# Kernel optimization log

Hardware: AMD Instinct MI355X
Metric: run time of the kernel (lower is better)

The kernel has to match this reference:

```python
import math
import jax, jax.numpy as jnp
import numpy as np

LOG2_E = math.log2(math.e)
C = 64          # channels
N = 150_000     # coarse-level occupied nodes
CHILD = 4       # occupied children per node (static => M is static)
M = N * CHILD   # fine-level points
K = 27          # 3x3x3 sparse-conv kernel offsets


def _prelu(x, a):
    return jnp.where(x >= 0, x, a * x)


def _sparse_conv(x, nbr, mask, W, b):
    """MinkowskiConvolution(k=3): y[i] = sum_k mask[i,k] * x[nbr[i,k]] @ W[k] + b.
    Fixed loop over K=27 offsets keeps peak memory at [n, C] per step."""
    y = jnp.zeros((x.shape[0], W.shape[2]), x.dtype)
    for k in range(W.shape[0]):
        g = x[nbr[:, k]] * mask[:, k, None]
        y = y + g @ W[k]
    return y + b


def setup_inputs() -> dict:
    rng = np.random.default_rng(0)
    # exactly CHILD occupied children per parent -> static M
    mask1 = np.argsort(rng.random((N, 8)), axis=1) < CHILD   # [N, 8] bool
    sel_idx = np.flatnonzero(mask1.reshape(-1)).astype(np.int32)  # [M]
    bins1_f = mask1.astype(np.float32)
    bins0 = rng.random((M, 8)) < 0.5
    bins0[:, 0] |= ~bins0.any(1)   # octree node has >=1 occupied child => label in [0,254]

    def nbrs(n):
        nb = rng.integers(0, n, size=(n, K)).astype(np.int32)
        mk = rng.random((n, K)) < 0.6
        nb[:, K // 2] = np.arange(n)  # center offset is self
        mk[:, K // 2] = True
        return nb, mk

    nbr0, mask0 = nbrs(N)
    nbr1, mask1k = nbrs(M)

    key = jax.random.key(0)
    ks = jax.random.split(key, 12)
    w = lambda k, sh, fan: (jax.random.normal(k, sh, jnp.float32) / np.sqrt(fan))
    params = dict(
        W_dec=w(ks[0], (C + 8, C), C + 8), b_dec=jnp.zeros((C,), jnp.float32), a_dec=jnp.float32(0.25),
        Wb1=w(ks[1], (K, C, C), K * C), bb1=jnp.zeros((C,), jnp.float32), ab1=jnp.float32(0.25),
        Wb2=w(ks[2], (K, C, C), K * C), bb2=jnp.zeros((C,), jnp.float32), ab2=jnp.float32(0.25),
        Wp0=w(ks[3], (K, C, C), K * C), bp0=jnp.zeros((C,), jnp.float32), ap0=jnp.float32(0.25),
        Wl0=w(ks[4], (C, 8 * C), C), bl0=jnp.zeros((8 * C,), jnp.float32),
        Wp1=w(ks[5], (K, C, C), K * C), bp1=jnp.zeros((C,), jnp.float32), ap1=jnp.float32(0.25),
        Wl1=w(ks[6], (C, 255), C), bl1=jnp.zeros((255,), jnp.float32),
    )
    return dict(
        cur_rec_F=jax.random.normal(ks[7], (N, C), jnp.float32),
        bins1_f=jnp.asarray(bins1_f), bins0=jnp.asarray(bins0),
        sel_idx=jnp.asarray(sel_idx),
        nbr0=jnp.asarray(nbr0), mask0=jnp.asarray(mask0),
        nbr1=jnp.asarray(nbr1), mask1=jnp.asarray(mask1k),
        points_num=M,
        **params,
    )


def reference(cur_rec_F, bins1_f, bins0, sel_idx, nbr0, mask0, nbr1, mask1, points_num,
              W_dec, b_dec, a_dec, Wb1, bb1, ab1, Wb2, bb2, ab2,
              Wp0, bp0, ap0, Wl0, bl0, Wp1, bp1, ap1, Wl1, bl1):
    # embed (pred_steps==2): identity on cur_bins[1].F
    embed_f = bins1_f                                   # [N, 8]
    # dec: Linear(C+8 -> C) + PReLU + Block(C)
    x = _prelu(jnp.concatenate([cur_rec_F, embed_f], 1) @ W_dec + b_dec, a_dec)
    h = _prelu(_sparse_conv(x, nbr0, mask0, Wb1, bb1), ab1)
    h = _sparse_conv(h, nbr0, mask0, Wb2, bb2) + x      # residual add (x.F.add_)
    rec = _prelu(h, ab2)                                # [N, C] -> cur_rec output
    # pred[0]: Conv3 + PReLU + Linear(C -> 8C)
    p = _prelu(_sparse_conv(rec, nbr0, mask0, Wp0, bp0), ap0)
    p = p @ Wl0 + bl0                                   # [N, 8C]
    # gather occupied children: reshape(N,8,C)[bins1] with static selection indices
    tmp = p.reshape(-1, p.shape[1] // 8)[sel_idx]       # [M, C]
    # pred[1] (last): Conv3 + PReLU + Linear(C -> 255) at finer stride
    q = _prelu(_sparse_conv(tmp, nbr1, mask1, Wp1, bp1), ap1)
    logits = q @ Wl1 + bl1                              # [M, 255]
    # bit-pack octree labels: (bins0 << arange(8)).sum(1) - 1
    oct = jnp.sum(bins0.astype(jnp.int32) * (1 << jnp.arange(8, dtype=jnp.int32)), 1) - 1
    logp = jax.nn.log_softmax(logits, axis=-1)
    ce = -jnp.take_along_axis(logp, oct[:, None], axis=1).sum()
    loss = ce * (LOG2_E / points_num)                   # batch_size==1 branch
    return rec, loss
```

## Files before the change

### kernel.cpp

```cpp
#include <hip/hip_runtime.h>
#include <hip/hip_bf16.h>

typedef __attribute__((ext_vector_type(8))) short bf16x8;
typedef __attribute__((ext_vector_type(4))) float f32x4;

#define MFMA(a,b,c) __builtin_amdgcn_mfma_f32_16x16x32_bf16(a,b,c,0,0,0)

__device__ __forceinline__ short f2b(float v){
  __hip_bfloat16 b = __float2bfloat16(v);
  return *reinterpret_cast<short*>(&b);
}
__device__ __forceinline__ float b2f(short s){
  __hip_bfloat16 b;
  *reinterpret_cast<short*>(&b) = s;
  return __bfloat162float(b);
}
__device__ __forceinline__ bool rd_mask(const void* m, long i, int flag){
  if (flag==1) return ((const int*)m)[i] != 0;
  if (flag==2) return ((const float*)m)[i] != 0.0f;
  return ((const unsigned char*)m)[i] != 0;
}

__device__ __forceinline__ void gld16(const void* g, void* l){
  __builtin_amdgcn_global_load_lds(
      (const __attribute__((address_space(1))) unsigned int*)g,
      (__attribute__((address_space(3))) unsigned int*)l, 16, 0, 0);
}
__device__ __forceinline__ void gld4(const void* g, void* l){
  __builtin_amdgcn_global_load_lds(
      (const __attribute__((address_space(1))) unsigned int*)g,
      (__attribute__((address_space(3))) unsigned int*)l, 4, 0, 0);
}

__global__ void k_detect(const void* __restrict__ mask, int* flag, float* ce,
                         int* zrow){
  int t = threadIdx.x;
  if (t < 32 && blockIdx.x==0) zrow[t] = 0;
  if (t==0 && blockIdx.x==0){
    const int* mi = (const int*)mask;
    const float* mf = (const float*)mask;
    bool all_i=true, all_f=true;
    for (int i=0;i<100;i++){
      if (mi[i*27+13] != 1) all_i=false;
      if (mf[i*27+13] != 1.0f) all_f=false;
    }
    *flag = all_i ? 1 : (all_f ? 2 : 0);
    *ce = 0.0f;
  }
}

__global__ __launch_bounds__(256) void k_merge(int* __restrict__ nbr,
    const void* __restrict__ mask, int total, const int* __restrict__ flagp){
  int flag = *flagp;
  int i = blockIdx.x*256 + threadIdx.x;
  if (i < total && !rd_mask(mask, i, flag)) nbr[i] = -1;
}

__global__ __launch_bounds__(256) void k_prep(
    const float* __restrict__ Wdec, const float* __restrict__ Wb1,
    const float* __restrict__ Wb2, const float* __restrict__ Wp0,
    const float* __restrict__ Wp1, const float* __restrict__ Wl0,
    const float* __restrict__ Wl1,
    short* __restrict__ wdecf, short* __restrict__ wconvf,
    short* __restrict__ wl0f, short* __restrict__ wl1f)
{
  int i = blockIdx.x*256 + threadIdx.x;
  if (i < 442368){
    int ci = i / 110592, r = i % 110592;
    int e = r&7, ln=(r>>3)&63, ks=(r>>9)&1, ct=(r>>10)&3, k=r>>12;
    int cin = ks*32 + (ln>>4)*8 + e, cout = ct*16 + (ln&15);
    const float* W = ci==0?Wb1: ci==1?Wb2: ci==2?Wp0:Wp1;
    wconvf[i] = f2b(W[(k*64+cin)*64 + cout]);
  } else if (i < 450560){
    int r = i - 442368;
    int e=r&7, ln=(r>>3)&63, ct=(r>>9)&3, ks=(r>>11)&3;
    int cin = ks*32 + (ln>>4)*8 + e, cout = ct*16 + (ln&15);
    wdecf[r] = f2b(cin<72 ? Wdec[cin*64+cout] : 0.f);
  } else if (i < 483328){
    int r = i - 450560;
    int e=r&7, ln=(r>>3)&63, ks=(r>>9)&1, ct=(r>>10)&3, cb=(r>>12)&7;
    int cin = ks*32+(ln>>4)*8+e, col = cb*64+ct*16+(ln&15);
    wl0f[r] = f2b(Wl0[cin*512 + col]);
  } else if (i < 499712){
    int r = i - 483328;
    int e=r&7, ln=(r>>3)&63, ks=(r>>9)&1, ct=(r>>10)&15;
    int cin = ks*32+(ln>>4)*8+e, col = ct*16+(ln&15);
    wl1f[r] = f2b(col<255 ? Wl1[cin*255+col] : 0.f);
  }
}

__global__ void k_inv_init(int* __restrict__ inv, int total){
  int i = blockIdx.x*256 + threadIdx.x;
  if (i < total) inv[i] = -1;
}
__global__ void k_inv_fill(const int* __restrict__ sel, int* __restrict__ inv, int M_){
  int m = blockIdx.x*256 + threadIdx.x;
  if (m < M_) inv[sel[m]] = m;
}

__global__ __launch_bounds__(256) void k_dec(
    const float* __restrict__ xf, const float* __restrict__ bf1,
    const short* __restrict__ wfrag, const float* __restrict__ bias,
    const float* __restrict__ alphap, short* __restrict__ outb, int n)
{
  __shared__ bf16x8 Au[2048];
  int t=threadIdx.x, lane=t&63, wid=t>>6;
  long row0 = (long)blockIdx.x*128;
  int sr=t>>1, sh=t&1;
  long r = row0+sr;
  bf16x8 u[8];
  #pragma unroll
  for (int j=0;j<8;j++) u[j] = bf16x8{0,0,0,0,0,0,0,0};
  if (r<n){
    if (sh==0){
      const f32x4* s = (const f32x4*)(xf + r*64);
      #pragma unroll
      for (int j=0;j<8;j++){
        f32x4 v0 = s[2*j], v1 = s[2*j+1];
        bf16x8 b;
        b[0]=f2b(v0[0]); b[1]=f2b(v0[1]); b[2]=f2b(v0[2]); b[3]=f2b(v0[3]);
        b[4]=f2b(v1[0]); b[5]=f2b(v1[1]); b[6]=f2b(v1[2]); b[7]=f2b(v1[3]);
        u[j]=b;
      }
    } else {
      const float* s = bf1 + r*8;
      bf16x8 b;
      #pragma unroll
      for (int j=0;j<8;j++) b[j]=f2b(s[j]);
      u[0]=b;
    }
  }
  int ub = sr*16 + sh*8;
  #pragma unroll
  for (int j=0;j<8;j++) Au[(ub+j)^(sr&7)] = u[j];
  __syncthreads();
  const bf16x8* wf = (const bf16x8*)wfrag;
  f32x4 acc[2][4];
  #pragma unroll
  for (int a_=0;a_<2;a_++)
  #pragma unroll
  for (int b_=0;b_<4;b_++) acc[a_][b_] = f32x4{0.f,0.f,0.f,0.f};
  #pragma unroll
  for (int ks=0;ks<4;ks++){
    bf16x8 a[2];
    #pragma unroll
    for (int rt=0;rt<2;rt++){
      int rr = wid*32 + rt*16 + (lane&15);
      a[rt] = Au[(rr*16 + ks*4 + (lane>>4)) ^ (rr&7)];
    }
    #pragma unroll
    for (int ct=0;ct<4;ct++){
      bf16x8 b = wf[(ks*4 + ct)*64 + lane];
      #pragma unroll
      for (int rt=0;rt<2;rt++) acc[rt][ct] = MFMA(a[rt], b, acc[rt][ct]);
    }
  }
  float al = alphap[0];
  #pragma unroll
  for (int rt=0;rt<2;rt++)
  #pragma unroll
  for (int ct=0;ct<4;ct++){
    int col = ct*16+(lane&15);
    float bc = bias[col];
    #pragma unroll
    for (int q=0;q<4;q++){
      long rr = row0 + wid*32 + rt*16 + (lane>>4)*4 + q;
      if (rr<n){
        float v = acc[rt][ct][q] + bc;
        v = v>=0.f? v : al*v;
        outb[rr*64+col] = f2b(v);
      }
    }
  }
}

__device__ __forceinline__ void conv_core(
    const short* __restrict__ xin, const int* __restrict__ nbrm,
    const short* __restrict__ wfrag, const short* __restrict__ zrow,
    short* As_, short* Bs_, int* Ns_,
    int n, int lane, int wid, long wrow0, f32x4 acc[2][4])
{
  auto issueA = [&](int slot, const int p[4]){
    short* dst = As_ + (wid*2 + slot)*2048;
    #pragma unroll
    for (int j=0;j<4;j++){
      int r = j*8 + (lane>>3);
      int s = (lane&7) ^ (r&7);
      const short* src = (p[j]<0) ? (zrow + s*8) : (xin + (long)p[j]*64 + s*8);
      gld16(src, dst + j*512);
    }
  };
  auto issueB = [&](int k){
    short* dst = Bs_ + (k&1)*4096 + wid*1024;
    #pragma unroll
    for (int j=0;j<2;j++)
      gld16(wfrag + ((long)k*512 + wid*128 + j*64 + lane)*8, dst + j*512);
  };
  auto issueN = [&](int k){
    int* dst = Ns_ + ((k&3)*4 + wid)*64;
    long R = wrow0 + (lane&31);
    if (R >= n) R = n-1;
    gld4(nbrm + R*27 + k, dst);
  };
  int p0[4], p1[4];
  #pragma unroll
  for (int j=0;j<4;j++){
    long R = wrow0 + j*8 + (lane>>3);
    bool v = R < n;
    long Rc = v ? R : (long)(n-1);
    p0[j] = v ? nbrm[Rc*27+0] : -1;
    p1[j] = v ? nbrm[Rc*27+1] : -1;
  }
  issueA(0, p0); __builtin_amdgcn_sched_barrier(0);
  issueN(2);     __builtin_amdgcn_sched_barrier(0);
  issueB(0);     __builtin_amdgcn_sched_barrier(0);
  issueA(1, p1); __builtin_amdgcn_sched_barrier(0);
  issueN(3);     __builtin_amdgcn_sched_barrier(0);
  #pragma unroll
  for (int k=0;k<27;k++){
    if (k<24)      asm volatile("s_waitcnt vmcnt(5)" ::: "memory");
    else if (k<26) asm volatile("s_waitcnt vmcnt(4)" ::: "memory");
    else           asm volatile("s_waitcnt vmcnt(0)" ::: "memory");
    __builtin_amdgcn_sched_barrier(0);
    __builtin_amdgcn_s_barrier();
    int pn[4];
    if (k<25){
      const int* sN = Ns_ + (((k+2)&3)*4 + wid)*64;
      #pragma unroll
      for (int j=0;j<4;j++) pn[j] = sN[j*8 + (lane>>3)];
    }
    bf16x8 a[2][2];
    const bf16x8* Aw = (const bf16x8*)(As_ + (wid*2 + (k&1))*2048);
    #pragma unroll
    for (int rt=0;rt<2;rt++){
      int r = rt*16 + (lane&15);
      #pragma unroll
      for (int h=0;h<2;h++)
        a[rt][h] = Aw[(r*8 + h*4 + (lane>>4)) ^ (r&7)];
    }
    bf16x8 b[4][2];
    const bf16x8* Bw = (const bf16x8*)(Bs_ + (k&1)*4096);
    #pragma unroll
    for (int ct=0;ct<4;ct++)
    #pragma unroll
    for (int h=0;h<2;h++)
      b[ct][h] = Bw[(ct*2+h)*64 + lane];
    asm volatile("s_waitcnt lgkmcnt(0)" ::: "memory");
    __builtin_amdgcn_sched_barrier(0);
    if (k<26){ issueB(k+1); __builtin_amdgcn_sched_barrier(0); }
    if (k<25){ issueA(k&1, pn); __builtin_amdgcn_sched_barrier(0); }
    if (k<23){ issueN(k+4); __builtin_amdgcn_sched_barrier(0); }
    #pragma unroll
    for (int ct=0;ct<4;ct++)
    #pragma unroll
    for (int h=0;h<2;h++){
      acc[0][ct] = MFMA(a[0][h], b[ct][h], acc[0][ct]);
      acc[1][ct] = MFMA(a[1][h], b[ct][h], acc[1][ct]);
    }
  }
}

__global__ __launch_bounds__(256,3) void k_conv(
    const short* __restrict__ xin, const int* __restrict__ nbrm,
    const short* __restrict__ wfrag, const float* __restrict__ bias,
    const float* __restrict__ alphap, const short* __restrict__ resid,
    short* __restrict__ outb, float* __restrict__ outf, int n,
    const short* __restrict__ zrow)
{
  __shared__ __align__(16) short As_[16384];
  __shared__ __align__(16) short Bs_[8192];
  __shared__ __align__(16) int   Ns_[1024];
  int t=threadIdx.x, lane=t&63, wid=t>>6;
  long wrow0 = (long)blockIdx.x*128 + wid*32;
  f32x4 acc[2][4];
  #pragma unroll
  for (int a_=0;a_<2;a_++)
  #pragma unroll
  for (int b_=0;b_<4;b_++) acc[a_][b_] = f32x4{0.f,0.f,0.f,0.f};
  conv_core(xin, nbrm, wfrag, zrow, As_, Bs_, Ns_, n, lane, wid, wrow0, acc);
  float al = alphap ? alphap[0] : 0.f;
  #pragma unroll
  for (int rt=0;rt<2;rt++)
  #pragma unroll
  for (int ct=0;ct<4;ct++){
    int col = ct*16 + (lane&15);
    float bc = bias[col];
    #pragma unroll
    for (int q=0;q<4;q++){
      long rr = wrow0 + rt*16 + (lane>>4)*4 + q;
      if (rr < n){
        float v = acc[rt][ct][q] + bc;
        if (resid) v += b2f(resid[rr*64+col]);
        if (alphap) v = v>=0.f ? v : al*v;
        outb[rr*64+col] = f2b(v);
        if (outf) outf[rr*64+col] = v;
      }
    }
  }
}

__global__ __launch_bounds__(256) void k_linscatter(
    const short* __restrict__ r0b, const short* __restrict__ wl0f,
    const float* __restrict__ bl0, const int* __restrict__ inv,
    short* __restrict__ tmpb, int n)
{
  __shared__ bf16x8 Au[1024];
  int t=threadIdx.x, lane=t&63, wid=t>>6, wrow=wid>>1, wcol=wid&1;
  long row0=(long)blockIdx.x*128;
  int sr=t>>1, sh=t&1;
  long r=row0+sr;
  bf16x8 z = {0,0,0,0,0,0,0,0};
  const bf16x8* s = (const bf16x8*)(r0b + r*64 + sh*32);
  int ub = sr*8+sh*4;
  #pragma unroll
  for (int j=0;j<4;j++) Au[(ub+j)^(sr&7)] = (r<n)? s[j] : z;
  __syncthreads();
  bf16x8 a[4][2];
  #pragma unroll
  for (int rt=0;rt<4;rt++){
    int rr = wrow*64 + rt*16 + (lane&15);
    #pragma unroll
    for (int ks=0;ks<2;ks++)
      a[rt][ks] = Au[(rr*8 + ks*4 + (lane>>4)) ^ (rr&7)];
  }
  const bf16x8* wf = (const bf16x8*)wl0f;
  for (int cb=0;cb<8;cb++){
    f32x4 acc[4][2];
    #pragma unroll
    for (int a_=0;a_<4;a_++)
    #pragma unroll
    for (int b_=0;b_<2;b_++) acc[a_][b_] = f32x4{0.f,0.f,0.f,0.f};
    #pragma unroll
    for (int ct=0;ct<2;ct++)
    #pragma unroll
    for (int ks=0;ks<2;ks++){
      bf16x8 b = wf[cb*512 + ((wcol*2+ct)*2+ks)*64 + lane];
      #pragma unroll
      for (int rt=0;rt<4;rt++) acc[rt][ct] = MFMA(a[rt][ks], b, acc[rt][ct]);
    }
    #pragma unroll
    for (int rt=0;rt<4;rt++)
    #pragma unroll
    for (int q=0;q<4;q++){
      long parent = row0 + wrow*64 + rt*16 + (lane>>4)*4 + q;
      if (parent < n){
        int m = inv[parent*8 + cb];
        if (m >= 0){
          #pragma unroll
          for (int ct=0;ct<2;ct++){
            int col = wcol*32 + ct*16 + (lane&15);
            tmpb[(long)m*64 + col] = f2b(acc[rt][ct][q] + bl0[cb*64+col]);
          }
        }
      }
    }
  }
}

__global__ __launch_bounds__(256,3) void k_convloss(
    const short* __restrict__ xin, const int* __restrict__ nbrm,
    const short* __restrict__ wfrag, const float* __restrict__ bias,
    const float* __restrict__ alphap, const short* __restrict__ wl1f,
    const float* __restrict__ bl1, const void* __restrict__ bins0,
    float* __restrict__ ce_out, int n, const int* __restrict__ flagp,
    const short* __restrict__ zrow)
{
  __shared__ __align__(16) short As_[16384];
  __shared__ __align__(16) short Bs_[8192];
  __shared__ __align__(16) int   Ns_[1024];
  int flag = *flagp;
  int t=threadIdx.x, lane=t&63, wid=t>>6;
  long wrow0 = (long)blockIdx.x*128 + wid*32;
  f32x4 acc[2][4];
  #pragma unroll
  for (int a_=0;a_<2;a_++)
  #pragma unroll
  for (int b_=0;b_<4;b_++) acc[a_][b_] = f32x4{0.f,0.f,0.f,0.f};
  conv_core(xin, nbrm, wfrag, zrow, As_, Bs_, Ns_, n, lane, wid, wrow0, acc);
  float al = alphap[0];
  short* Qs = As_ + (wid*2)*2048;
  #pragma unroll
  for (int rt=0;rt<2;rt++)
  #pragma unroll
  for (int ct=0;ct<4;ct++){
    int col = ct*16 + (lane&15);
    float bc = bias[col];
    #pragma unroll
    for (int q=0;q<4;q++){
      int lrow = rt*16 + (lane>>4)*4 + q;
      float v = acc[rt][ct][q] + bc;
      v = v>=0.f ? v : al*v;
      Qs[(lrow*8 + ((col>>3)^(lrow&7)))*8 + (col&7)] = f2b(v);
    }
  }
  const bf16x8* wl = (const bf16x8*)wl1f;
  const bf16x8* Qw = (const bf16x8*)Qs;
  float ce_local = 0.f;
  int c0=lane&15, gq=lane>>4;
  #pragma unroll
  for (int rt=0; rt<2; rt++){
    int rr = rt*16 + (lane&15);
    bf16x8 a0 = Qw[(rr*8 + (lane>>4)) ^ (rr&7)];
    bf16x8 a1 = Qw[(rr*8 + 4 + (lane>>4)) ^ (rr&7)];
    f32x4 acl[16];
    #pragma unroll
    for (int ct=0;ct<16;ct++) acl[ct]=f32x4{0.f,0.f,0.f,0.f};
    #pragma unroll
    for (int ct=0;ct<16;ct++){
      acl[ct]=MFMA(a0, wl[(ct*2)*64+lane],   acl[ct]);
      acl[ct]=MFMA(a1, wl[(ct*2+1)*64+lane], acl[ct]);
    }
    #pragma unroll
    for (int q=0;q<4;q++){
      long rowg = wrow0 + rt*16 + gq*4 + q;
      bool valid = rowg < (long)n;
      int oct=-1;
      if (valid){
        #pragma unroll
        for (int j=0;j<8;j++) if (rd_mask(bins0, rowg*8+j, flag)) oct += (1<<j);
      }
      float lg[16]; float mx=-3e38f;
      #pragma unroll
      for (int ct=0;ct<16;ct++){
        int col=ct*16+c0;
        float v = acl[ct][q] + ((col<255)? bl1[col] : -1e30f);
        lg[ct]=v; mx=fmaxf(mx,v);
      }
      #pragma unroll
      for (int d=1; d<16; d<<=1) mx = fmaxf(mx, __shfl_xor(mx,d));
      float sm=0.f, selv=0.f;
      #pragma unroll
      for (int ct=0;ct<16;ct++){
        sm += __expf(lg[ct]-mx);
        if (valid && ct==(oct>>4) && c0==(oct&15)) selv=lg[ct];
      }
      #pragma unroll
      for (int d=1; d<16; d<<=1) sm += __shfl_xor(sm,d);
      if (valid && c0==(oct&15)) ce_local += mx + __logf(sm) - selv;
    }
  }
  #pragma unroll
  for (int d=1; d<64; d<<=1) ce_local += __shfl_xor(ce_local,d);
  if (lane==0) atomicAdd(ce_out, ce_local);
}

__global__ void k_final(const float* __restrict__ ce, float* __restrict__ out, float scale){
  if (threadIdx.x==0 && blockIdx.x==0) out[0] = ce[0]*scale;
}

extern "C" void kernel_launch(void* const* d_in, const int* in_sizes, int n_in,
                              void* d_out, int out_size, void* d_ws, size_t ws_size,
                              hipStream_t stream) {
  const int N = in_sizes[0] / 64;
  const int M = in_sizes[3];
  char* ws = (char*)d_ws;
  int*   flag = (int*)ws;
  float* ce   = (float*)(ws + 64);
  short* zrow = (short*)(ws + 128);
  short* wconvf = (short*)(ws + 256);
  short* wb1f = wconvf;
  short* wb2f = wb1f + 110592;
  short* wp0f = wb2f + 110592;
  short* wp1f = wp0f + 110592;
  short* wdecf= wp1f + 110592;
  short* wl0f = wdecf + 8192;
  short* wl1f = wl0f + 32768;
  int*   inv  = (int*)(ws + ((size_t)1<<20));
  size_t off_act = (((size_t)1<<20) + (size_t)N*8*4 + 4095) & ~(size_t)4095;
  short* xb   = (short*)(ws + off_act);
  short* h1b  = xb + (size_t)N*64;
  short* recb = h1b + (size_t)N*64;
  short* r0b  = xb;
  short* tmpb = h1b;

  int* nbr0 = (int*)d_in[4];
  int* nbr1 = (int*)d_in[6];
  const float* a_dec = (const float*)d_in[11];
  int gN = (N+127)/128, gM = (M+127)/128;

  k_detect<<<1,64,0,stream>>>(d_in[5], flag, ce, (int*)zrow);
  k_merge<<<(N*27+255)/256,256,0,stream>>>(nbr0, d_in[5], N*27, flag);
  k_merge<<<(M*27+255)/256,256,0,stream>>>(nbr1, d_in[7], M*27, flag);
  k_prep<<<1952,256,0,stream>>>(
      (const float*)d_in[9], (const float*)d_in[12], (const float*)d_in[15],
      (const float*)d_in[18], (const float*)d_in[23], (const float*)d_in[21],
      (const float*)d_in[26], wdecf, wconvf, wl0f, wl1f);
  k_inv_init<<<(N*8+255)/256,256,0,stream>>>(inv, N*8);
  k_inv_fill<<<(M+255)/256,256,0,stream>>>((const int*)d_in[3], inv, M);
  k_dec<<<gN,256,0,stream>>>((const float*)d_in[0], (const float*)d_in[1], wdecf,
      (const float*)d_in[10], a_dec, xb, N);
  k_conv<<<gN,256,0,stream>>>(xb, nbr0, wb1f,
      (const float*)d_in[13], (const float*)d_in[14], nullptr, h1b, nullptr, N, zrow);
  k_conv<<<gN,256,0,stream>>>(h1b, nbr0, wb2f,
      (const float*)d_in[16], (const float*)d_in[17], xb, recb, (float*)d_out, N, zrow);
  k_conv<<<gN,256,0,stream>>>(recb, nbr0, wp0f,
      (const float*)d_in[19], (const float*)d_in[20], nullptr, r0b, nullptr, N, zrow);
  k_linscatter<<<gN,256,0,stream>>>(r0b, wl0f, (const float*)d_in[22], inv, tmpb, N);
  k_convloss<<<gM,256,0,stream>>>(tmpb, nbr1, wp1f,
      (const float*)d_in[24], (const float*)d_in[25], wl1f, (const float*)d_in[27],
      d_in[2], ce, M, flag, zrow);
  float scale = 1.4426950408889634f / (float)M;
  k_final<<<1,64,0,stream>>>(ce, (float*)d_out + (size_t)N*64, scale);
}
```

Baseline: 1.076 ms.

## Load conv weights into registers, drop block barriers, use zero-row sentinel

Conv weight fragments now go from global memory straight into double-buffered VGPRs instead of being staged through shared memory. This removes the per-offset workgroup barrier, since each wave only reads its own LDS slot, and it frees LDS so occupancy can rise from 3 to 4 blocks per CU. Masked neighbours are redirected to a zeroed extra row at index n, so gather addresses are formed with plain unsigned arithmetic and no branch. Each wave now reads the full weight tile itself, which multiplies L2 weight traffic by four. The extra weight registers also put pressure on the raised occupancy target.

```diff
diff --git a/kernel.cpp b/kernel.cpp
--- a/kernel.cpp
+++ b/kernel.cpp
@@ -5,6 +5,7 @@
 typedef __attribute__((ext_vector_type(4))) float f32x4;
 
 #define MFMA(a,b,c) __builtin_amdgcn_mfma_f32_16x16x32_bf16(a,b,c,0,0,0)
+#define SB() __builtin_amdgcn_sched_barrier(0)
 
 __device__ __forceinline__ short f2b(float v){
   __hip_bfloat16 b = __float2bfloat16(v);
@@ -32,11 +33,8 @@
       (__attribute__((address_space(3))) unsigned int*)l, 4, 0, 0);
 }
 
-__global__ void k_detect(const void* __restrict__ mask, int* flag, float* ce,
-                         int* zrow){
-  int t = threadIdx.x;
-  if (t < 32 && blockIdx.x==0) zrow[t] = 0;
-  if (t==0 && blockIdx.x==0){
+__global__ void k_detect(const void* __restrict__ mask, int* flag, float* ce){
+  if (threadIdx.x==0 && blockIdx.x==0){
     const int* mi = (const int*)mask;
     const float* mf = (const float*)mask;
     bool all_i=true, all_f=true;
@@ -49,11 +47,17 @@
   }
 }
 
+__global__ void k_zero(short* a, short* b, short* c, short* d){
+  int t = threadIdx.x, w = t>>6, cc = t&63;
+  if (w==0) a[cc]=0; else if (w==1) b[cc]=0; else if (w==2) c[cc]=0; else d[cc]=0;
+}
+
 __global__ __launch_bounds__(256) void k_merge(int* __restrict__ nbr,
-    const void* __restrict__ mask, int total, const int* __restrict__ flagp){
+    const void* __restrict__ mask, int total, const int* __restrict__ flagp,
+    int zidx){
   int flag = *flagp;
   int i = blockIdx.x*256 + threadIdx.x;
-  if (i < total && !rd_mask(mask, i, flag)) nbr[i] = -1;
+  if (i < total && !rd_mask(mask, i, flag)) nbr[i] = zidx;
 }
 
 __global__ __launch_bounds__(256) void k_prep(
@@ -176,108 +180,111 @@
 
 __device__ __forceinline__ void conv_core(
     const short* __restrict__ xin, const int* __restrict__ nbrm,
-    const short* __restrict__ wfrag, const short* __restrict__ zrow,
-    short* As_, short* Bs_, int* Ns_,
-    int n, int lane, int wid, long wrow0, f32x4 acc[2][4])
+    const short* __restrict__ wfrag,
+    short* As_, int* Ns_,
+    int n, int lane, int wid, int wrow0, f32x4 acc[2][4])
 {
-  auto issueA = [&](int slot, const int p[4]){
+  bf16x8 breg[2][8];
+  const char* wb = (const char*)wfrag;
+  unsigned sw16 = (unsigned)(((lane&7) ^ (lane>>3))*16);
+  auto loadB = [&](int k, int s){
+    #pragma unroll
+    for (int j=0;j<8;j++){
+      unsigned voff = (unsigned)((k*512 + j*64 + lane)*16);
+      asm volatile("global_load_dwordx4 %0, %1, %2"
+        : "=v"(breg[s][j]) : "v"(voff), "s"(wb) : "memory");
+    }
+  };
+  auto issueA = [&](int slot, const unsigned va[4]){
     short* dst = As_ + (wid*2 + slot)*2048;
     #pragma unroll
-    for (int j=0;j<4;j++){
-      int r = j*8 + (lane>>3);
-      int s = (lane&7) ^ (r&7);
-      const short* src = (p[j]<0) ? (zrow + s*8) : (xin + (long)p[j]*64 + s*8);
-      gld16(src, dst + j*512);
-    }
-  };
-  auto issueB = [&](int k){
-    short* dst = Bs_ + (k&1)*4096 + wid*1024;
-    #pragma unroll
-    for (int j=0;j<2;j++)
-      gld16(wfrag + ((long)k*512 + wid*128 + j*64 + lane)*8, dst + j*512);
+    for (int j=0;j<4;j++)
+      gld16((const char*)xin + va[j], dst + j*512);
   };
   auto issueN = [&](int k){
     int* dst = Ns_ + ((k&3)*4 + wid)*64;
-    long R = wrow0 + (lane&31);
+    int R = wrow0 + (lane&31);
     if (R >= n) R = n-1;
-    gld4(nbrm + R*27 + k, dst);
+    gld4(nbrm + (long)R*27 + k, dst);
   };
-  int p0[4], p1[4];
+  unsigned va0[4], va1[4];
   #pragma unroll
   for (int j=0;j<4;j++){
-    long R = wrow0 + j*8 + (lane>>3);
+    int R = wrow0 + j*8 + (lane>>3);
     bool v = R < n;
-    long Rc = v ? R : (long)(n-1);
-    p0[j] = v ? nbrm[Rc*27+0] : -1;
-    p1[j] = v ? nbrm[Rc*27+1] : -1;
-  }
-  issueA(0, p0); __builtin_amdgcn_sched_barrier(0);
-  issueN(2);     __builtin_amdgcn_sched_barrier(0);
-  issueB(0);     __builtin_amdgcn_sched_barrier(0);
-  issueA(1, p1); __builtin_amdgcn_sched_barrier(0);
-  issueN(3);     __builtin_amdgcn_sched_barrier(0);
+    int Rc = v ? R : 0;
+    int p0 = v ? nbrm[(long)Rc*27+0] : n;
+    int p1 = v ? nbrm[(long)Rc*27+1] : n;
+    va0[j] = (unsigned)p0*128u + sw16;
+    va1[j] = (unsigned)p1*128u + sw16;
+  }
+  SB();
+  loadB(0,0);    SB();
+  issueA(0,va0); SB();
+  issueN(2);     SB();
+  issueA(1,va1); SB();
+  issueN(3);     SB();
   #pragma unroll
   for (int k=0;k<27;k++){
     if (k<24)      asm volatile("s_waitcnt vmcnt(5)" ::: "memory");
     else if (k<26) asm volatile("s_waitcnt vmcnt(4)" ::: "memory");
     else           asm volatile("s_waitcnt vmcnt(0)" ::: "memory");
-    __builtin_amdgcn_sched_barrier(0);
-    __builtin_amdgcn_s_barrier();
-    int pn[4];
+    SB();
+    unsigned van[4];
     if (k<25){
       const int* sN = Ns_ + (((k+2)&3)*4 + wid)*64;
       #pragma unroll
-      for (int j=0;j<4;j++) pn[j] = sN[j*8 + (lane>>3)];
-    }
-    bf16x8 a[2][2];
+      for (int j=0;j<4;j++)
+        van[j] = (unsigned)sN[j*8 + (lane>>3)]*128u + sw16;
+    }
+    if (k<26){ loadB(k+1, (k+1)&1); SB(); }
     const bf16x8* Aw = (const bf16x8*)(As_ + (wid*2 + (k&1))*2048);
-    #pragma unroll
-    for (int rt=0;rt<2;rt++){
-      int r = rt*16 + (lane&15);
-      #pragma unroll
-      for (int h=0;h<2;h++)
-        a[rt][h] = Aw[(r*8 + h*4 + (lane>>4)) ^ (r&7)];
-    }
-    bf16x8 b[4][2];
-    const bf16x8* Bw = (const bf16x8*)(Bs_ + (k&1)*4096);
-    #pragma unroll
-    for (int ct=0;ct<4;ct++)
-    #pragma unroll
-    for (int h=0;h<2;h++)
-      b[ct][h] = Bw[(ct*2+h)*64 + lane];
+    bf16x8 a0, a1;
+    {
+      int r = (lane&15);
+      a0 = Aw[(r*8 + (lane>>4)) ^ (r&7)];
+      a1 = Aw[(r*8 + 4 + (lane>>4)) ^ (r&7)];
+    }
     asm volatile("s_waitcnt lgkmcnt(0)" ::: "memory");
-    __builtin_amdgcn_sched_barrier(0);
-    if (k<26){ issueB(k+1); __builtin_amdgcn_sched_barrier(0); }
-    if (k<25){ issueA(k&1, pn); __builtin_amdgcn_sched_barrier(0); }
-    if (k<23){ issueN(k+4); __builtin_amdgcn_sched_barrier(0); }
-    #pragma unroll
-    for (int ct=0;ct<4;ct++)
-    #pragma unroll
-    for (int h=0;h<2;h++){
-      acc[0][ct] = MFMA(a[0][h], b[ct][h], acc[0][ct]);
-      acc[1][ct] = MFMA(a[1][h], b[ct][h], acc[1][ct]);
-    }
-  }
-}
-
-__global__ __launch_bounds__(256,3) void k_conv(
+    SB();
+    #pragma unroll
+    for (int ct=0;ct<4;ct++){
+      acc[0][ct] = MFMA(a0, breg[k&1][ct*2+0], acc[0][ct]);
+      acc[0][ct] = MFMA(a1, breg[k&1][ct*2+1], acc[0][ct]);
+    }
+    {
+      int r = 16 + (lane&15);
+      a0 = Aw[(r*8 + (lane>>4)) ^ (r&7)];
+      a1 = Aw[(r*8 + 4 + (lane>>4)) ^ (r&7)];
+    }
+    asm volatile("s_waitcnt lgkmcnt(0)" ::: "memory");
+    SB();
+    if (k<25){ issueA(k&1, van); SB(); }
+    if (k<23){ issueN(k+4); SB(); }
+    #pragma unroll
+    for (int ct=0;ct<4;ct++){
+      acc[1][ct] = MFMA(a0, breg[k&1][ct*2+0], acc[1][ct]);
+      acc[1][ct] = MFMA(a1, breg[k&1][ct*2+1], acc[1][ct]);
+    }
+  }
+}
+
+__global__ __launch_bounds__(256,4) void k_conv(
     const short* __restrict__ xin, const int* __restrict__ nbrm,
     const short* __restrict__ wfrag, const float* __restrict__ bias,
     const float* __restrict__ alphap, const short* __restrict__ resid,
-    short* __restrict__ outb, float* __restrict__ outf, int n,
-    const short* __restrict__ zrow)
+    short* __restrict__ outb, float* __restrict__ outf, int n)
 {
   __shared__ __align__(16) short As_[16384];
-  __shared__ __align__(16) short Bs_[8192];
   __shared__ __align__(16) int   Ns_[1024];
   int t=threadIdx.x, lane=t&63, wid=t>>6;
-  long wrow0 = (long)blockIdx.x*128 + wid*32;
+  int wrow0 = blockIdx.x*128 + wid*32;
   f32x4 acc[2][4];
   #pragma unroll
   for (int a_=0;a_<2;a_++)
   #pragma unroll
   for (int b_=0;b_<4;b_++) acc[a_][b_] = f32x4{0.f,0.f,0.f,0.f};
-  conv_core(xin, nbrm, wfrag, zrow, As_, Bs_, Ns_, n, lane, wid, wrow0, acc);
+  conv_core(xin, nbrm, wfrag, As_, Ns_, n, lane, wid, wrow0, acc);
   float al = alphap ? alphap[0] : 0.f;
   #pragma unroll
   for (int rt=0;rt<2;rt++)
@@ -287,7 +294,7 @@
     float bc = bias[col];
     #pragma unroll
     for (int q=0;q<4;q++){
-      long rr = wrow0 + rt*16 + (lane>>4)*4 + q;
+      long rr = (long)wrow0 + rt*16 + (lane>>4)*4 + q;
       if (rr < n){
         float v = acc[rt][ct][q] + bc;
         if (resid) v += b2f(resid[rr*64+col]);
@@ -357,26 +364,24 @@
   }
 }
 
-__global__ __launch_bounds__(256,3) void k_convloss(
+__global__ __launch_bounds__(256,4) void k_convloss(
     const short* __restrict__ xin, const int* __restrict__ nbrm,
     const short* __restrict__ wfrag, const float* __restrict__ bias,
     const float* __restrict__ alphap, const short* __restrict__ wl1f,
     const float* __restrict__ bl1, const void* __restrict__ bins0,
-    float* __restrict__ ce_out, int n, const int* __restrict__ flagp,
-    const short* __restrict__ zrow)
+    float* __restrict__ ce_out, int n, const int* __restrict__ flagp)
 {
   __shared__ __align__(16) short As_[16384];
-  __shared__ __align__(16) short Bs_[8192];
   __shared__ __align__(16) int   Ns_[1024];
   int flag = *flagp;
   int t=threadIdx.x, lane=t&63, wid=t>>6;
-  long wrow0 = (long)blockIdx.x*128 + wid*32;
+  int wrow0 = blockIdx.x*128 + wid*32;
   f32x4 acc[2][4];
   #pragma unroll
   for (int a_=0;a_<2;a_++)
   #pragma unroll
   for (int b_=0;b_<4;b_++) acc[a_][b_] = f32x4{0.f,0.f,0.f,0.f};
-  conv_core(xin, nbrm, wfrag, zrow, As_, Bs_, Ns_, n, lane, wid, wrow0, acc);
+  conv_core(xin, nbrm, wfrag, As_, Ns_, n, lane, wid, wrow0, acc);
   float al = alphap[0];
   short* Qs = As_ + (wid*2)*2048;
   #pragma unroll
@@ -393,6 +398,7 @@
       Qs[(lrow*8 + ((col>>3)^(lrow&7)))*8 + (col&7)] = f2b(v);
     }
   }
+  __builtin_amdgcn_s_barrier();
   const bf16x8* wl = (const bf16x8*)wl1f;
   const bf16x8* Qw = (const bf16x8*)Qs;
   float ce_local = 0.f;
@@ -412,7 +418,7 @@
     }
     #pragma unroll
     for (int q=0;q<4;q++){
-      long rowg = wrow0 + rt*16 + gq*4 + q;
+      long rowg = (long)wrow0 + rt*16 + gq*4 + q;
       bool valid = rowg < (long)n;
       int oct=-1;
       if (valid){
@@ -456,7 +462,6 @@
   char* ws = (char*)d_ws;
   int*   flag = (int*)ws;
   float* ce   = (float*)(ws + 64);
-  short* zrow = (short*)(ws + 128);
   short* wconvf = (short*)(ws + 256);
   short* wb1f = wconvf;
   short* wb2f = wb1f + 110592;
@@ -468,8 +473,8 @@
   int*   inv  = (int*)(ws + ((size_t)1<<20));
   size_t off_act = (((size_t)1<<20) + (size_t)N*8*4 + 4095) & ~(size_t)4095;
   short* xb   = (short*)(ws + off_act);
-  short* h1b  = xb + (size_t)N*64;
-  short* recb = h1b + (size_t)N*64;
+  short* h1b  = xb + (size_t)(N+1)*64;
+  short* recb = h1b + (size_t)(N+1)*64;
   short* r0b  = xb;
   short* tmpb = h1b;
 
@@ -478,9 +483,11 @@
   const float* a_dec = (const float*)d_in[11];
   int gN = (N+127)/128, gM = (M+127)/128;
 
-  k_detect<<<1,64,0,stream>>>(d_in[5], flag, ce, (int*)zrow);
-  k_merge<<<(N*27+255)/256,256,0,stream>>>(nbr0, d_in[5], N*27, flag);
-  k_merge<<<(M*27+255)/256,256,0,stream>>>(nbr1, d_in[7], M*27, flag);
+  k_detect<<<1,64,0,stream>>>(d_in[5], flag, ce);
+  k_zero<<<1,256,0,stream>>>(xb + (size_t)N*64, h1b + (size_t)N*64,
+                             recb + (size_t)N*64, tmpb + (size_t)M*64);
+  k_merge<<<(N*27+255)/256,256,0,stream>>>(nbr0, d_in[5], N*27, flag, N);
+  k_merge<<<(M*27+255)/256,256,0,stream>>>(nbr1, d_in[7], M*27, flag, M);
   k_prep<<<1952,256,0,stream>>>(
       (const float*)d_in[9], (const float*)d_in[12], (const float*)d_in[15],
       (const float*)d_in[18], (const float*)d_in[23], (const float*)d_in[21],
@@ -490,15 +497,15 @@
   k_dec<<<gN,256,0,stream>>>((const float*)d_in[0], (const float*)d_in[1], wdecf,
       (const float*)d_in[10], a_dec, xb, N);
   k_conv<<<gN,256,0,stream>>>(xb, nbr0, wb1f,
-      (const float*)d_in[13], (const float*)d_in[14], nullptr, h1b, nullptr, N, zrow);
+      (const float*)d_in[13], (const float*)d_in[14], nullptr, h1b, nullptr, N);
   k_conv<<<gN,256,0,stream>>>(h1b, nbr0, wb2f,
-      (const float*)d_in[16], (const float*)d_in[17], xb, recb, (float*)d_out, N, zrow);
+      (const float*)d_in[16], (const float*)d_in[17], xb, recb, (float*)d_out, N);
   k_conv<<<gN,256,0,stream>>>(recb, nbr0, wp0f,
-      (const float*)d_in[19], (const float*)d_in[20], nullptr, r0b, nullptr, N, zrow);
+      (const float*)d_in[19], (const float*)d_in[20], nullptr, r0b, nullptr, N);
   k_linscatter<<<gN,256,0,stream>>>(r0b, wl0f, (const float*)d_in[22], inv, tmpb, N);
   k_convloss<<<gM,256,0,stream>>>(tmpb, nbr1, wp1f,
       (const float*)d_in[24], (const float*)d_in[25], wl1f, (const float*)d_in[27],
-      d_in[2], ce, M, flag, zrow);
+      d_in[2], ce, M, flag);
   float scale = 1.4426950408889634f / (float)M;
   k_final<<<1,64,0,stream>>>(ce, (float*)d_out + (size_t)N*64, scale);
 }
```

Result: slower. 1.257 ms (+16.8%).
